# Performance work log

Measured on AMD Instinct MI355X. Metric: run time of the kernel, lower is better.

The kernel has to match this reference:

```python
import jax, jax.numpy as jnp
import numpy as np

B, C, H, W = 8, 256, 64, 64
GROUPS = 32
EPS = 1e-5


def setup_inputs() -> dict:
    key = jax.random.key(0)
    ks = jax.random.split(key, 6)
    s = 1.0 / np.sqrt(C)
    return {
        "x": jax.random.normal(ks[0], (B, C, H, W), dtype=jnp.float32),
        "gn_w": jnp.ones((C,), jnp.float32),
        "gn_b": jnp.zeros((C,), jnp.float32),
        "wq": jax.random.normal(ks[1], (C, C), jnp.float32) * s,
        "bq": jnp.zeros((C,), jnp.float32),
        "wk": jax.random.normal(ks[2], (C, C), jnp.float32) * s,
        "bk": jnp.zeros((C,), jnp.float32),
        "wv": jax.random.normal(ks[3], (C, C), jnp.float32) * s,
        "bv": jnp.zeros((C,), jnp.float32),
        "wo": jax.random.normal(ks[4], (C, C), jnp.float32) * s,
        "bo": jnp.zeros((C,), jnp.float32),
    }


def group_norm(x, w, b):
    # x: [B, C, H, W]; normalize over (C//GROUPS, H, W) per group
    Bn, Cn, Hn, Wn = x.shape
    xg = x.reshape(Bn, GROUPS, Cn // GROUPS, Hn, Wn)
    mu = jnp.mean(xg, axis=(2, 3, 4), keepdims=True)
    var = jnp.var(xg, axis=(2, 3, 4), keepdims=True)
    xn = (xg - mu) * jax.lax.rsqrt(var + EPS)
    xn = xn.reshape(Bn, Cn, Hn, Wn)
    return xn * w[None, :, None, None] + b[None, :, None, None]


def reference(x, gn_w, gn_b, wq, bq, wk, bk, wv, bv, wo, bo):
    Bn, Cn, Hn, Wn = x.shape
    h = group_norm(x, gn_w, gn_b)
    hf = h.reshape(Bn, Cn, Hn * Wn)  # [B, C, N]
    # 1x1 conv == channel matmul; produce tokens-major [B, N, C]
    q = jnp.einsum('bcn,oc->bno', hf, wq) + bq  # [B, N, C]
    k = jnp.einsum('bcn,oc->bon', hf, wk) + bk[None, :, None]  # [B, C, N]
    v = jnp.einsum('bcn,oc->bno', hf, wv) + bv  # [B, N, C]
    alpha = jnp.einsum('bnc,bcm->bnm', q, k) / jnp.sqrt(jnp.float32(Cn))
    alpha = jax.nn.softmax(alpha, axis=-1)  # [B, N, N]
    out = jnp.einsum('bnm,bmc->bnc', alpha, v)  # [B, N, C]
    out = jnp.einsum('bnc,oc->bon', out, wo) + bo[None, :, None]  # [B, C, N]
    return out.reshape(Bn, Cn, Hn, Wn) + x
```

## Files before the change

kernel.cpp:

```cpp
#include <hip/hip_runtime.h>
#include <hip/hip_bf16.h>
#include <cstdint>


typedef short short8 __attribute__((ext_vector_type(8)));
typedef float f32x16 __attribute__((ext_vector_type(16)));

__device__ __forceinline__ unsigned short f2bf(float f){
  uint32_t u = __builtin_bit_cast(uint32_t, f);
  u += 0x7FFFu + ((u >> 16) & 1u);
  return (unsigned short)(u >> 16);
}
__device__ __forceinline__ uint32_t pk2t(float a, float b){
  return (__builtin_bit_cast(uint32_t,a)>>16) | (__builtin_bit_cast(uint32_t,b)&0xFFFF0000u);
}
__device__ __forceinline__ void gload16(const void* g, void* l){
  auto gp = reinterpret_cast<uint32_t __attribute__((address_space(1)))*>(
      reinterpret_cast<uintptr_t>(g));
  auto lp = reinterpret_cast<uint32_t __attribute__((address_space(3)))*>(
      reinterpret_cast<uintptr_t>(l));
  __builtin_amdgcn_global_load_lds(gp, lp, 16, 0, 0);
}
__device__ __forceinline__ float xmax32(float x){ return fmaxf(x, __shfl_xor(x,32)); }
__device__ __forceinline__ float xsum32(float x){ return x + __shfl_xor(x,32); }

__global__ void cvt_w_kernel(const float* wq, const float* wk, const float* wv, const float* wo,
                             ushort* wqb, ushort* wkb, ushort* wvb, ushort* wob){
  int i = blockIdx.x*256 + threadIdx.x;
  wqb[i]=f2bf(wq[i]); wkb[i]=f2bf(wk[i]); wvb[i]=f2bf(wv[i]); wob[i]=f2bf(wo[i]);
}

__global__ void gn_stats1_kernel(const float* __restrict__ x, float* __restrict__ part){
  int blk = blockIdx.x;
  const float* p = x + (size_t)(blk>>3)*32768 + (blk&7)*4096;
  float s=0.f, sq=0.f;
  #pragma unroll
  for(int j=0;j<4;j++){
    float4 v = *reinterpret_cast<const float4*>(p + threadIdx.x*16 + j*4);
    s += v.x+v.y+v.z+v.w;
    sq += v.x*v.x+v.y*v.y+v.z*v.z+v.w*v.w;
  }
  #pragma unroll
  for(int o=32;o>0;o>>=1){ s+=__shfl_down(s,o); sq+=__shfl_down(sq,o); }
  __shared__ float ls[4], lq[4];
  if((threadIdx.x&63)==0){ ls[threadIdx.x>>6]=s; lq[threadIdx.x>>6]=sq; }
  __syncthreads();
  if(threadIdx.x==0){
    part[blk*2]  =ls[0]+ls[1]+ls[2]+ls[3];
    part[blk*2+1]=lq[0]+lq[1]+lq[2]+lq[3];
  }
}
__global__ void gn_stats2_kernel(const float* __restrict__ part, float* __restrict__ gst){
  int bg = threadIdx.x;
  float s=0.f, sq=0.f;
  #pragma unroll
  for(int j=0;j<8;j++){ s+=part[(bg*8+j)*2]; sq+=part[(bg*8+j)*2+1]; }
  float mu=s*(1.f/32768.f);
  float var=sq*(1.f/32768.f)-mu*mu;
  gst[bg*2]=mu; gst[bg*2+1]=rsqrtf(var+1e-5f);
}

__global__ void gn_apply_kernel(const float* __restrict__ x, const float* __restrict__ gw,
                                const float* __restrict__ gb, const float* __restrict__ gst,
                                ushort* __restrict__ ht){
  int nt=blockIdx.x, ct=blockIdx.y, b=blockIdx.z;
  int n0=nt*64, c0=ct*32;
  __shared__ float tile[32][65];
  __shared__ float smu[4], srs[4], sw[32], sb[32];
  int tid=threadIdx.x;
  if(tid<4){ int g=(c0>>3)+tid; smu[tid]=gst[(b*32+g)*2]; srs[tid]=gst[(b*32+g)*2+1]; }
  if(tid<32){ sw[tid]=gw[c0+tid]; sb[tid]=gb[c0+tid]; }
  __syncthreads();
  int ci=tid>>3, j0=(tid&7)*8;
  const float* xp = x + ((size_t)(b*256)+c0+ci)*4096 + n0 + j0;
  float mu=smu[ci>>3], rs=srs[ci>>3], w=sw[ci], bb=sb[ci];
  float4 va=*reinterpret_cast<const float4*>(xp);
  float4 vb=*reinterpret_cast<const float4*>(xp+4);
  tile[ci][j0+0]=(va.x-mu)*rs*w+bb; tile[ci][j0+1]=(va.y-mu)*rs*w+bb;
  tile[ci][j0+2]=(va.z-mu)*rs*w+bb; tile[ci][j0+3]=(va.w-mu)*rs*w+bb;
  tile[ci][j0+4]=(vb.x-mu)*rs*w+bb; tile[ci][j0+5]=(vb.y-mu)*rs*w+bb;
  tile[ci][j0+6]=(vb.z-mu)*rs*w+bb; tile[ci][j0+7]=(vb.w-mu)*rs*w+bb;
  __syncthreads();
  int nl=tid>>2, oct=tid&3;
  union{ ushort u[8]; uint4 v; } o;
  #pragma unroll
  for(int j=0;j<8;j++) o.u[j]=f2bf(tile[oct*8+j][nl]);
  *reinterpret_cast<uint4*>(ht + ((size_t)(b*4096)+n0+nl)*256 + c0 + oct*8) = o.v;
}

__global__ __launch_bounds__(256,2) void gemm_qk(const ushort* __restrict__ A,
         const ushort* __restrict__ Bq, const ushort* __restrict__ Bk,
         ushort* __restrict__ Dq, ushort* __restrict__ Dk,
         const float* __restrict__ bq, const float* __restrict__ bk, float qscale){
  __shared__ ushort Al[128*64];
  __shared__ ushort Bql[128*64];
  __shared__ ushort Bkl[128*64];
  int m0=blockIdx.x*128, n0=blockIdx.y*128;
  int tid=threadIdx.x, w=tid>>6, lane=tid&63, ln=lane&31, hi=lane>>5;
  f32x16 aq[2][2], ak[2][2];
  #pragma unroll
  for(int a=0;a<2;a++)
    #pragma unroll
    for(int c=0;c<2;c++)
      #pragma unroll
      for(int r=0;r<16;r++){ aq[a][c][r]=0.f; ak[a][c][r]=0.f; }
  for(int kt=0;kt<4;kt++){
    __syncthreads();
    #pragma unroll
    for(int i=0;i<4;i++){
      int idx=i*256+tid; int row=idx>>3; int chs=(idx^row)&7;
      gload16(A  + (size_t)(m0+row)*256 + kt*64 + chs*8, (char*)Al  + (i*256+w*64)*16);
    }
    #pragma unroll
    for(int i=0;i<4;i++){
      int idx=i*256+tid; int row=idx>>3; int chs=(idx^row)&7;
      gload16(Bq + (size_t)(n0+row)*256 + kt*64 + chs*8, (char*)Bql + (i*256+w*64)*16);
    }
    #pragma unroll
    for(int i=0;i<4;i++){
      int idx=i*256+tid; int row=idx>>3; int chs=(idx^row)&7;
      gload16(Bk + (size_t)(n0+row)*256 + kt*64 + chs*8, (char*)Bkl + (i*256+w*64)*16);
    }
    __syncthreads();
    #pragma unroll
    for(int kk=0;kk<4;kk++){
      short8 af[2], bqf[2], bkf[2];
      #pragma unroll
      for(int t=0;t<2;t++){
        int ra=(w>>1)*64+t*32+ln; int ca=((kk*2+hi)^ra)&7;
        af[t]=*reinterpret_cast<const short8*>(Al + ra*64 + ca*8);
        int rb=(w&1)*64+t*32+ln; int cb=((kk*2+hi)^rb)&7;
        bqf[t]=*reinterpret_cast<const short8*>(Bql + rb*64 + cb*8);
        bkf[t]=*reinterpret_cast<const short8*>(Bkl + rb*64 + cb*8);
      }
      #pragma unroll
      for(int ti=0;ti<2;ti++)
        #pragma unroll
        for(int tj=0;tj<2;tj++){
          aq[ti][tj]=__builtin_amdgcn_mfma_f32_32x32x16_bf16(af[ti],bqf[tj],aq[ti][tj],0,0,0);
          ak[ti][tj]=__builtin_amdgcn_mfma_f32_32x32x16_bf16(af[ti],bkf[tj],ak[ti][tj],0,0,0);
        }
    }
  }
  #pragma unroll
  for(int ti=0;ti<2;ti++){
    #pragma unroll
    for(int tj=0;tj<2;tj++){
      int col=n0+(w&1)*64+tj*32+ln;
      float bqc=bq[col], bkc=bk[col];
      #pragma unroll
      for(int r=0;r<16;r++){
        int row=m0+(w>>1)*64+ti*32+(r&3)+8*(r>>2)+4*hi;
        Dq[(size_t)row*256+col]=f2bf((aq[ti][tj][r]+bqc)*qscale);
        Dk[(size_t)row*256+col]=f2bf(ak[ti][tj][r]+bkc);
      }
    }
  }
}

__global__ __launch_bounds__(256,2) void gemm_vt(const ushort* __restrict__ A, const ushort* __restrict__ Bm,
         ushort* __restrict__ D, const float* __restrict__ bias){
  __shared__ ushort Al[128*64];
  __shared__ ushort Bl[128*64];
  int m0=blockIdx.x*128, n0=blockIdx.y*128;
  int tid=threadIdx.x, w=tid>>6, lane=tid&63, ln=lane&31, hi=lane>>5;
  f32x16 acc[2][2];
  #pragma unroll
  for(int a=0;a<2;a++)
    #pragma unroll
    for(int c=0;c<2;c++)
      #pragma unroll
      for(int r=0;r<16;r++) acc[a][c][r]=0.f;
  for(int kt=0;kt<4;kt++){
    __syncthreads();
    #pragma unroll
    for(int i=0;i<4;i++){
      int idx=i*256+tid; int row=idx>>3; int chs=(idx^row)&7;
      gload16(A + (size_t)(m0+row)*256 + kt*64 + chs*8, (char*)Al + (i*256+w*64)*16);
    }
    #pragma unroll
    for(int i=0;i<4;i++){
      int idx=i*256+tid; int row=idx>>3; int chs=(idx^row)&7;
      gload16(Bm + (size_t)(n0+row)*256 + kt*64 + chs*8, (char*)Bl + (i*256+w*64)*16);
    }
    __syncthreads();
    #pragma unroll
    for(int kk=0;kk<4;kk++){
      short8 af[2], bfr[2];
      #pragma unroll
      for(int t=0;t<2;t++){
        int ra=(w>>1)*64+t*32+ln; int ca=((kk*2+hi)^ra)&7;
        af[t]=*reinterpret_cast<const short8*>(Al + ra*64 + ca*8);
        int rb=(w&1)*64+t*32+ln; int cb=((kk*2+hi)^rb)&7;
        bfr[t]=*reinterpret_cast<const short8*>(Bl + rb*64 + cb*8);
      }
      #pragma unroll
      for(int ti=0;ti<2;ti++)
        #pragma unroll
        for(int tj=0;tj<2;tj++)
          acc[ti][tj]=__builtin_amdgcn_mfma_f32_32x32x16_bf16(af[ti],bfr[tj],acc[ti][tj],0,0,0);
    }
  }
  #pragma unroll
  for(int ti=0;ti<2;ti++){
    #pragma unroll
    for(int tj=0;tj<2;tj++){
      int col=n0+(w&1)*64+tj*32+ln;
      #pragma unroll
      for(int r=0;r<16;r++){
        int row=m0+(w>>1)*64+ti*32+(r&3)+8*(r>>2)+4*hi;
        D[(size_t)row*32768+col]=f2bf(acc[ti][tj][r]+bias[row]);
      }
    }
  }
}

__global__ __launch_bounds__(256,2) void attn_kernel(
    const ushort* __restrict__ qb, const ushort* __restrict__ kb,
    const ushort* __restrict__ vtb, const ushort* __restrict__ wob,
    const float* __restrict__ bo, const float* __restrict__ x,
    float* __restrict__ out){
  __shared__ ushort Kl[64*256];
  __shared__ ushort Vl[256*64];
  __shared__ float ml[4][2][32];
  float* exch = reinterpret_cast<float*>(Kl);
  int tid=threadIdx.x, w=tid>>6, lane=tid&63, ln=lane&31, hi=lane>>5;
  int qg=w&1, h=w>>1;
  int bid=blockIdx.x;
  int cid=(bid&7)*64 + (bid>>3);
  int b=cid>>6, nt=cid&63;
  int n0=nt*64+qg*32;
  int n=n0+ln;
  short8 qf[16];
  {
    const ushort* qrow = qb + ((size_t)(b*4096)+n)*256 + hi*8;
    #pragma unroll
    for(int kc=0;kc<16;kc++) qf[kc]=*reinterpret_cast<const short8*>(qrow+kc*16);
  }
  f32x16 oacc[8];
  #pragma unroll
  for(int i=0;i<8;i++)
    #pragma unroll
    for(int r=0;r<16;r++) oacc[i][r]=0.f;
  float M=-3.0e38f, L=0.f;
  const ushort* kbp = kb + (size_t)b*4096*256;
  const ushort* vbp = vtb + (size_t)b*4096;

  auto stageK=[&](int t1){
    #pragma unroll
    for(int i=0;i<8;i++){
      int idx=i*256+tid; int row=idx>>5, ch=idx&31;
      int chs=(ch&24)|((ch^row)&7);
      gload16(kbp + (size_t)(t1*64+row)*256 + chs*8, (char*)Kl + (i*256+w*64)*16);
    }
  };
  auto stageV=[&](int t1){
    #pragma unroll
    for(int i=0;i<8;i++){
      int idx=i*256+tid; int row=idx>>3; int chs=(idx^row)&7;
      gload16(vbp + (size_t)row*32768 + t1*64 + chs*8, (char*)Vl + (i*256+w*64)*16);
    }
  };

  stageK(0); stageV(0);

  for(int t=0;t<64;t++){
    asm volatile("s_waitcnt vmcnt(8)" ::: "memory");
    asm volatile("s_barrier" ::: "memory");
    f32x16 s;
    #pragma unroll
    for(int r=0;r<16;r++) s[r]=0.f;
    int kr=h*32+ln;
    const ushort* klr = Kl + kr*256;
    #pragma unroll
    for(int kc=0;kc<16;kc++){
      int cw=kc*2+hi; int chs=(cw&24)|((cw^kr)&7);
      short8 a=*reinterpret_cast<const short8*>(klr+chs*8);
      s=__builtin_amdgcn_mfma_f32_32x32x16_bf16(a,qf[kc],s,0,0,0);
    }
    asm volatile("s_barrier" ::: "memory");
    if(t<63) stageK(t+1);
    float tmax=fmaxf(fmaxf(fmaxf(s[0],s[1]),fmaxf(s[2],s[3])),
                     fmaxf(fmaxf(s[4],s[5]),fmaxf(s[6],s[7])));
    float tmax2=fmaxf(fmaxf(fmaxf(s[8],s[9]),fmaxf(s[10],s[11])),
                      fmaxf(fmaxf(s[12],s[13]),fmaxf(s[14],s[15])));
    tmax=xmax32(fmaxf(tmax,tmax2));
    if(__any(tmax > M + 8.f)){
      float Mn=fmaxf(M,tmax);
      float sc=exp2f(M-Mn);
      L*=sc;
      #pragma unroll
      for(int i=0;i<8;i++)
        #pragma unroll
        for(int r=0;r<16;r++) oacc[i][r]*=sc;
      M=Mn;
    }
    float p[16]; float ts=0.f;
    #pragma unroll
    for(int r=0;r<16;r++){ p[r]=exp2f(s[r]-M); ts+=p[r]; }
    L+=xsum32(ts);
    short8 pa[2];
    #pragma unroll
    for(int ks=0;ks<2;ks++){
      uint32_t c01=pk2t(p[ks*8+0],p[ks*8+1]);
      uint32_t c23=pk2t(p[ks*8+2],p[ks*8+3]);
      uint32_t c45=pk2t(p[ks*8+4],p[ks*8+5]);
      uint32_t c67=pk2t(p[ks*8+6],p[ks*8+7]);
      uint32_t x01=(uint32_t)__shfl_xor((int)c01,32), x23=(uint32_t)__shfl_xor((int)c23,32);
      uint32_t x45=(uint32_t)__shfl_xor((int)c45,32), x67=(uint32_t)__shfl_xor((int)c67,32);
      union{ uint32_t u[4]; short8 v; } r_;
      r_.u[0]= hi? x45:c01;
      r_.u[1]= hi? x67:c23;
      r_.u[2]= hi? c45:x01;
      r_.u[3]= hi? c67:x23;
      pa[ks]=r_.v;
    }
    if(t<63){ asm volatile("s_waitcnt vmcnt(8)" ::: "memory"); }
    else    { asm volatile("s_waitcnt vmcnt(0)" ::: "memory"); }
    asm volatile("s_barrier" ::: "memory");
    #pragma unroll
    for(int ct=0;ct<8;ct++){
      int c=ct*32+ln;
      const ushort* vlr = Vl + c*64;
      #pragma unroll
      for(int ks=0;ks<2;ks++){
        int cw=h*4+ks*2+hi; int chs=cw^(c&7);
        short8 a=*reinterpret_cast<const short8*>(vlr+chs*8);
        oacc[ct]=__builtin_amdgcn_mfma_f32_32x32x16_bf16(a,pa[ks],oacc[ct],0,0,0);
      }
    }
    asm volatile("s_barrier" ::: "memory");
    if(t<63) stageV(t+1);
  }
  __syncthreads();
  if(hi==0){ ml[w][0][ln]=M; ml[w][1][ln]=L; }
  __syncthreads();
  float Mp=ml[w^2][0][ln], Lp=ml[w^2][1][ln];
  float Mt=fmaxf(M,Mp);
  float fo=exp2f(M-Mt), fpp=exp2f(Mp-Mt);
  float g=fo/(fo*L+fpp*Lp);
  #pragma unroll
  for(int i=0;i<8;i++)
    #pragma unroll
    for(int r=0;r<16;r++) oacc[i][r]*=g;
  short8 obf[16];
  #pragma unroll
  for(int cb=0;cb<4;cb++){
    __syncthreads();
    float* ex=exch + w*2048;
    #pragma unroll
    for(int u=0;u<2;u++){
      int ct=cb*2+u;
      #pragma unroll
      for(int r=0;r<16;r++){
        int cl=u*32+(r&3)+8*(r>>2)+4*hi;
        ex[cl*32+ln]=oacc[ct][r];
      }
    }
    __syncthreads();
    const float* exq=exch + (w^2)*2048;
    #pragma unroll
    for(int u=0;u<2;u++){
      int ct=cb*2+u;
      #pragma unroll
      for(int r=0;r<16;r++){
        int cl=u*32+(r&3)+8*(r>>2)+4*hi;
        oacc[ct][r]+=exq[cl*32+ln];
      }
    }
    #pragma unroll
    for(int kq=0;kq<4;kq++){
      int ct=cb*2+(kq>>1); int rb=(kq&1)*8;
      uint32_t c01=pk2t(oacc[ct][rb+0],oacc[ct][rb+1]);
      uint32_t c23=pk2t(oacc[ct][rb+2],oacc[ct][rb+3]);
      uint32_t c45=pk2t(oacc[ct][rb+4],oacc[ct][rb+5]);
      uint32_t c67=pk2t(oacc[ct][rb+6],oacc[ct][rb+7]);
      uint32_t x01=(uint32_t)__shfl_xor((int)c01,32), x23=(uint32_t)__shfl_xor((int)c23,32);
      uint32_t x45=(uint32_t)__shfl_xor((int)c45,32), x67=(uint32_t)__shfl_xor((int)c67,32);
      union{ uint32_t u[4]; short8 v; } r_;
      r_.u[0]= hi? x45:c01;
      r_.u[1]= hi? x67:c23;
      r_.u[2]= hi? c45:x01;
      r_.u[3]= hi? c67:x23;
      obf[cb*4+kq]=r_.v;
    }
  }
  #pragma unroll
  for(int cot=0;cot<4;cot++){
    f32x16 d;
    #pragma unroll
    for(int r=0;r<16;r++) d[r]=0.f;
    int coa=h*128+cot*32+ln;
    const ushort* wr=wob+(size_t)coa*256+hi*8;
    #pragma unroll
    for(int kbv=0;kbv<16;kbv++){
      short8 a=*reinterpret_cast<const short8*>(wr+kbv*16);
      d=__builtin_amdgcn_mfma_f32_32x32x16_bf16(a,obf[kbv],d,0,0,0);
    }
    #pragma unroll
    for(int r=0;r<16;r++){
      int co=h*128+cot*32+(r&3)+8*(r>>2)+4*hi;
      size_t oi=((size_t)(b*256)+co)*4096 + n0+ln;
      out[oi]=d[r]+bo[co]+x[oi];
    }
  }
}

extern "C" void kernel_launch(void* const* d_in, const int* in_sizes, int n_in,
                              void* d_out, int out_size, void* d_ws, size_t ws_size,
                              hipStream_t stream){
  const float* x   =(const float*)d_in[0];
  const float* gw  =(const float*)d_in[1];
  const float* gb  =(const float*)d_in[2];
  const float* wq  =(const float*)d_in[3];
  const float* bq  =(const float*)d_in[4];
  const float* wk  =(const float*)d_in[5];
  const float* bk  =(const float*)d_in[6];
  const float* wv  =(const float*)d_in[7];
  const float* bv  =(const float*)d_in[8];
  const float* wo  =(const float*)d_in[9];
  const float* bo  =(const float*)d_in[10];
  float* out=(float*)d_out;
  char* ws=(char*)d_ws;
  const size_t SZ = (size_t)32768*256*2;
  ushort* ht =(ushort*)(ws);
  ushort* qb =(ushort*)(ws+SZ);
  ushort* kb2=(ushort*)(ws+2*SZ);
  ushort* vtb=(ushort*)(ws+3*SZ);
  ushort* wqb=(ushort*)(ws+4*SZ);
  ushort* wkb=(ushort*)(ws+4*SZ+131072);
  ushort* wvb=(ushort*)(ws+4*SZ+262144);
  ushort* wob=(ushort*)(ws+4*SZ+393216);
  float*  gst=(float*) (ws+4*SZ+524288);
  float*  part=(float*)(ws+4*SZ+524288+2048);

  cvt_w_kernel<<<256,256,0,stream>>>(wq,wk,wv,wo,wqb,wkb,wvb,wob);
  gn_stats1_kernel<<<2048,256,0,stream>>>(x,part);
  gn_stats2_kernel<<<1,256,0,stream>>>(part,gst);
  gn_apply_kernel<<<dim3(64,8,8),256,0,stream>>>(x,gw,gb,gst,ht);
  gemm_qk<<<dim3(256,2),256,0,stream>>>(ht,wqb,wkb,qb,kb2,bq,bk,0.090168439f);
  gemm_vt<<<dim3(2,256),256,0,stream>>>(wvb,ht,vtb,bv);
  attn_kernel<<<512,256,0,stream>>>(qb,kb2,vtb,wob,bo,x,out);
}
```

Baseline: 342.2 us.

## Double-buffer K/V tiles in attention and widen block to 128 queries

The attention kernel now runs 512 threads per block over 128 query rows, so one staged K/V tile is shared by twice as many queries. K and V are kept in two LDS buffers each, and the next tile's loads are issued at the top of each iteration, before the current tile is used. This replaces the old scheme of staging after barriers on a single buffer. LDS use grows to about 128 KB per block, which limits each CU to one resident block, and the grid shrinks to 256 blocks. The K swizzle becomes a full 5-bit XOR, and the cross-wave partner for combining softmax partials changes to w^4.

```diff
diff --git a/kernel.cpp b/kernel.cpp
--- a/kernel.cpp
+++ b/kernel.cpp
@@ -215,21 +215,21 @@
   }
 }
 
-__global__ __launch_bounds__(256,2) void attn_kernel(
+__global__ __launch_bounds__(512,2) void attn_kernel(
     const ushort* __restrict__ qb, const ushort* __restrict__ kb,
     const ushort* __restrict__ vtb, const ushort* __restrict__ wob,
     const float* __restrict__ bo, const float* __restrict__ x,
     float* __restrict__ out){
-  __shared__ ushort Kl[64*256];
-  __shared__ ushort Vl[256*64];
-  __shared__ float ml[4][2][32];
-  float* exch = reinterpret_cast<float*>(Kl);
+  __shared__ ushort Kl[2][64*256];
+  __shared__ ushort Vl[2][256*64];
+  __shared__ float ml[8][2][32];
+  float* exch = reinterpret_cast<float*>(&Kl[0][0]);
   int tid=threadIdx.x, w=tid>>6, lane=tid&63, ln=lane&31, hi=lane>>5;
-  int qg=w&1, h=w>>1;
+  int qg=w&3, h=w>>2;
   int bid=blockIdx.x;
-  int cid=(bid&7)*64 + (bid>>3);
-  int b=cid>>6, nt=cid&63;
-  int n0=nt*64+qg*32;
+  int cid=(bid&7)*32 + (bid>>3);
+  int b=cid>>5, nt=cid&31;
+  int n0=nt*128+qg*32;
   int n=n0+ln;
   short8 qf[16];
   {
@@ -246,40 +246,45 @@
   const ushort* kbp = kb + (size_t)b*4096*256;
   const ushort* vbp = vtb + (size_t)b*4096;
 
-  auto stageK=[&](int t1){
-    #pragma unroll
-    for(int i=0;i<8;i++){
-      int idx=i*256+tid; int row=idx>>5, ch=idx&31;
-      int chs=(ch&24)|((ch^row)&7);
-      gload16(kbp + (size_t)(t1*64+row)*256 + chs*8, (char*)Kl + (i*256+w*64)*16);
+  auto stageK=[&](int t1, int bi){
+    #pragma unroll
+    for(int i=0;i<4;i++){
+      int idx=i*512+tid; int row=idx>>5, ch=idx&31;
+      int chs=ch^(row&31);
+      gload16(kbp + (size_t)(t1*64+row)*256 + chs*8, (char*)&Kl[bi][0] + (i*512+w*64)*16);
     }
   };
-  auto stageV=[&](int t1){
-    #pragma unroll
-    for(int i=0;i<8;i++){
-      int idx=i*256+tid; int row=idx>>3; int chs=(idx^row)&7;
-      gload16(vbp + (size_t)row*32768 + t1*64 + chs*8, (char*)Vl + (i*256+w*64)*16);
+  auto stageV=[&](int t1, int bi){
+    #pragma unroll
+    for(int i=0;i<4;i++){
+      int idx=i*512+tid; int row=idx>>3; int chs=(idx^row)&7;
+      gload16(vbp + (size_t)row*32768 + t1*64 + chs*8, (char*)&Vl[bi][0] + (i*512+w*64)*16);
     }
   };
 
-  stageK(0); stageV(0);
+  stageK(0,0); stageV(0,0);
 
   for(int t=0;t<64;t++){
-    asm volatile("s_waitcnt vmcnt(8)" ::: "memory");
+    int cur=t&1;
+    if(t<63){
+      stageK(t+1,cur^1);
+      stageV(t+1,cur^1);
+      asm volatile("s_waitcnt vmcnt(24)" ::: "memory");
+    } else {
+      asm volatile("s_waitcnt vmcnt(8)" ::: "memory");
+    }
     asm volatile("s_barrier" ::: "memory");
     f32x16 s;
     #pragma unroll
     for(int r=0;r<16;r++) s[r]=0.f;
     int kr=h*32+ln;
-    const ushort* klr = Kl + kr*256;
+    const ushort* klr = &Kl[cur][0] + kr*256;
     #pragma unroll
     for(int kc=0;kc<16;kc++){
-      int cw=kc*2+hi; int chs=(cw&24)|((cw^kr)&7);
+      int cw=kc*2+hi; int chs=cw^(kr&31);
       short8 a=*reinterpret_cast<const short8*>(klr+chs*8);
       s=__builtin_amdgcn_mfma_f32_32x32x16_bf16(a,qf[kc],s,0,0,0);
     }
-    asm volatile("s_barrier" ::: "memory");
-    if(t<63) stageK(t+1);
     float tmax=fmaxf(fmaxf(fmaxf(s[0],s[1]),fmaxf(s[2],s[3])),
                      fmaxf(fmaxf(s[4],s[5]),fmaxf(s[6],s[7])));
     float tmax2=fmaxf(fmaxf(fmaxf(s[8],s[9]),fmaxf(s[10],s[11])),
@@ -315,13 +320,13 @@
       r_.u[3]= hi? c67:x23;
       pa[ks]=r_.v;
     }
-    if(t<63){ asm volatile("s_waitcnt vmcnt(8)" ::: "memory"); }
-    else    { asm volatile("s_waitcnt vmcnt(0)" ::: "memory"); }
+    if(t<63){ asm volatile("s_waitcnt vmcnt(16)" ::: "memory"); }
+    else    { asm volatile("s_waitcnt vmcnt(0)"  ::: "memory"); }
     asm volatile("s_barrier" ::: "memory");
     #pragma unroll
     for(int ct=0;ct<8;ct++){
       int c=ct*32+ln;
-      const ushort* vlr = Vl + c*64;
+      const ushort* vlr = &Vl[cur][0] + c*64;
       #pragma unroll
       for(int ks=0;ks<2;ks++){
         int cw=h*4+ks*2+hi; int chs=cw^(c&7);
@@ -330,12 +335,11 @@
       }
     }
     asm volatile("s_barrier" ::: "memory");
-    if(t<63) stageV(t+1);
   }
   __syncthreads();
   if(hi==0){ ml[w][0][ln]=M; ml[w][1][ln]=L; }
   __syncthreads();
-  float Mp=ml[w^2][0][ln], Lp=ml[w^2][1][ln];
+  float Mp=ml[w^4][0][ln], Lp=ml[w^4][1][ln];
   float Mt=fmaxf(M,Mp);
   float fo=exp2f(M-Mt), fpp=exp2f(Mp-Mt);
   float g=fo/(fo*L+fpp*Lp);
@@ -358,7 +362,7 @@
       }
     }
     __syncthreads();
-    const float* exq=exch + (w^2)*2048;
+    const float* exq=exch + (w^4)*2048;
     #pragma unroll
     for(int u=0;u<2;u++){
       int ct=cb*2+u;
@@ -440,5 +444,5 @@
   gn_apply_kernel<<<dim3(64,8,8),256,0,stream>>>(x,gw,gb,gst,ht);
   gemm_qk<<<dim3(256,2),256,0,stream>>>(ht,wqb,wkb,qb,kb2,bq,bk,0.090168439f);
   gemm_vt<<<dim3(2,256),256,0,stream>>>(wvb,ht,vtb,bv);
-  attn_kernel<<<512,256,0,stream>>>(qb,kb2,vtb,wob,bo,x,out);
-}
+  attn_kernel<<<256,512,0,stream>>>(qb,kb2,vtb,wob,bo,x,out);
+}
```

After: 325.0 us. 1.05x faster.
